# Kernel optimization log

Measured on AMD Instinct MI355X. Metric: run time of the kernel, lower is better.

## Reference

```python
import jax, jax.numpy as jnp
import numpy as np

B, S, D = 32, 512, 768
EPS = 1e-8  # torch CosineSimilarity eps

def setup_inputs() -> dict:
    key = jax.random.key(0)
    k1, k2, k3, k4 = jax.random.split(key, 4)
    emb1 = jax.random.normal(k1, (B, S, D), jnp.float32)
    emb2 = jax.random.normal(k2, (B, S, D), jnp.float32)
    mask1 = jax.random.randint(k3, (B, S), 0, 2).astype(jnp.int32)
    mask2 = jax.random.randint(k4, (B, S), 0, 2).astype(jnp.int32)
    return {"emb1": emb1, "emb2": emb2, "mask1": mask1, "mask2": mask2}

def reference(emb1, emb2, mask1, mask2):
    # normalize token embeddings (cosine sim = dot of unit vectors)
    n1 = emb1 / jnp.maximum(jnp.linalg.norm(emb1, axis=-1, keepdims=True), EPS)
    n2 = emb2 / jnp.maximum(jnp.linalg.norm(emb2, axis=-1, keepdims=True), EPS)
    # full pairwise cosine similarity: [B, S1, S2]
    sim = jnp.einsum('bid,bjd->bij', n1, n2)
    m1 = mask1.astype(sim.dtype)
    m2 = mask2.astype(sim.dtype)
    valid = m1[:, :, None] * m2[:, None, :]
    neg_inf = jnp.asarray(-jnp.inf, sim.dtype)
    masked = jnp.where(valid > 0, sim, neg_inf)
    # row max over valid cols; rows with no valid token contribute 0
    row_max = jnp.where(m1 > 0, jnp.max(masked, axis=2), 0.0)  # [B, S1]
    col_max = jnp.where(m2 > 0, jnp.max(masked, axis=1), 0.0)  # [B, S2]
    denom = jnp.sum(m1, axis=1) + jnp.sum(m2, axis=1)          # n1 + n2
    score = (jnp.sum(row_max, axis=1) + jnp.sum(col_max, axis=1)) / jnp.maximum(denom, 1.0)
    return score  # [B]
```

## Files before the change

kernel.cpp:

```cpp
#include <hip/hip_runtime.h>

#define BB 32
#define SS 512
#define DD 768
#define NROW (BB * SS)

typedef float f32x4 __attribute__((ext_vector_type(4)));
typedef short bf16x8 __attribute__((ext_vector_type(8)));

__device__ __forceinline__ unsigned fkey(float f) {
  unsigned u = __float_as_uint(f);
  return (u & 0x80000000u) ? ~u : (u | 0x80000000u);
}
__device__ __forceinline__ float fdecode(unsigned k) {
  return __uint_as_float((k & 0x80000000u) ? (k & 0x7fffffffu) : ~k);
}
__device__ __forceinline__ unsigned short cvt_bf16(float f) {
  unsigned u = __float_as_uint(f);
  u += 0x7fffu + ((u >> 16) & 1u);
  return (unsigned short)(u >> 16);
}

__global__ __launch_bounds__(64) void index_kernel(
    const int* __restrict__ mask1, const int* __restrict__ mask2,
    int* __restrict__ idx1, int* __restrict__ idx2,
    int* __restrict__ nt1, int* __restrict__ nt2,
    unsigned* __restrict__ rowkey, unsigned* __restrict__ colkey) {
  int side = blockIdx.x & 1, b = blockIdx.x >> 1;
  const int* m = (side ? mask2 : mask1) + b * SS;
  unsigned* key = (side ? colkey : rowkey) + b * SS;
  int* idx = (side ? idx2 : idx1) + b * SS;
  int l = threadIdx.x;
  int nv = 0, lastelem = 0;
#pragma unroll
  for (int c = 0; c < 8; ++c) {
    int e = c * 64 + l;
    int v = m[e];
    key[e] = 0x007fffffu;
    unsigned long long bal = __ballot(v != 0);
    int pos = nv + __popcll(bal & ((1ull << l) - 1ull));
    if (v) idx[pos] = e;
    nv += __popcll(bal);
    if (bal) lastelem = c * 64 + (63 - __clzll(bal));
  }
  int nt = (nv + 127) >> 7;
  for (int p = nv + l; p < nt * 128; p += 64) idx[p] = lastelem;
  if (l == 0) (side ? nt2 : nt1)[b] = nt;
}

__global__ __launch_bounds__(256) void norm_cvt_kernel(
    const float* __restrict__ emb1, const float* __restrict__ emb2,
    const int* __restrict__ mask1, const int* __restrict__ mask2,
    unsigned short* __restrict__ wsA, unsigned short* __restrict__ wsB) {
  int wave = blockIdx.x * 4 + (threadIdx.x >> 6);
  int lane = threadIdx.x & 63;
  int half = wave >> 14;
  int r = wave & (NROW - 1);
  if ((half ? mask2 : mask1)[r] == 0) return;
  const float* src = (half ? emb2 : emb1) + (size_t)r * DD;
  float4 v[3];
  float s = 0.f;
#pragma unroll
  for (int q = 0; q < 3; ++q) {
    v[q] = ((const float4*)src)[q * 64 + lane];
    s += v[q].x * v[q].x + v[q].y * v[q].y + v[q].z * v[q].z + v[q].w * v[q].w;
  }
#pragma unroll
  for (int m = 1; m < 64; m <<= 1) s += __shfl_xor(s, m);
  float inv = 1.0f / fmaxf(sqrtf(s), 1e-8f);
  unsigned short* dst = (half ? wsB : wsA) + (size_t)r * DD;
#pragma unroll
  for (int q = 0; q < 3; ++q) {
    ushort4 u;
    u.x = cvt_bf16(v[q].x * inv); u.y = cvt_bf16(v[q].y * inv);
    u.z = cvt_bf16(v[q].z * inv); u.w = cvt_bf16(v[q].w * inv);
    *(ushort4*)(dst + q * 256 + lane * 4) = u;
  }
}

__global__ __launch_bounds__(256) void simmax_kernel(
    const unsigned short* __restrict__ wsA, const unsigned short* __restrict__ wsB,
    const int* __restrict__ idx1, const int* __restrict__ idx2,
    const int* __restrict__ nt1, const int* __restrict__ nt2,
    unsigned* __restrict__ rowkey, unsigned* __restrict__ colkey) {
  int x = blockIdx.x;
  int b = x & 31;
  int tile = x >> 5;
  int ti = tile >> 2, tj = tile & 3;
  if (ti >= nt1[b] || tj >= nt2[b]) return;
  int i0 = ti << 7, j0 = tj << 7;
  __shared__ __align__(16) unsigned short sA[2][128 * 64];
  __shared__ __align__(16) unsigned short sB[2][128 * 64];
  int t = threadIdx.x, l = t & 63, wid = t >> 6, wr = wid >> 1, wc = wid & 1;
  int rsub = l >> 3, csub = l & 7;
  int ra[4], rb[4];
#pragma unroll
  for (int j = 0; j < 4; ++j) {
    int rowblk = (wid * 4 + j) * 8;
    ra[j] = idx1[b * SS + i0 + rowblk + rsub];
    rb[j] = idx2[b * SS + j0 + rowblk + rsub];
  }
  const unsigned short* gA = wsA + (size_t)b * SS * DD;
  const unsigned short* gB = wsB + (size_t)b * SS * DD;
  int csw = (csub ^ rsub) << 3;

  f32x4 acc[4][4] = {};

#define STAGE(buf, k0)                                                              \
  {                                                                                 \
    _Pragma("unroll") for (int j = 0; j < 4; ++j) {                                 \
      int rowblk = (wid * 4 + j) * 8;                                               \
      const unsigned short* ga = gA + (size_t)ra[j] * DD + (k0) + csw;              \
      const unsigned short* gb = gB + (size_t)rb[j] * DD + (k0) + csw;              \
      __builtin_amdgcn_global_load_lds(                                             \
          (const __attribute__((address_space(1))) unsigned int*)ga,                \
          (__attribute__((address_space(3))) unsigned int*)&sA[buf][rowblk * 64],   \
          16, 0, 0);                                                                \
      __builtin_amdgcn_global_load_lds(                                             \
          (const __attribute__((address_space(1))) unsigned int*)gb,                \
          (__attribute__((address_space(3))) unsigned int*)&sB[buf][rowblk * 64],   \
          16, 0, 0);                                                                \
    }                                                                               \
  }

  STAGE(0, 0);
  __syncthreads();
  int cur = 0;
#pragma unroll 1
  for (int tk = 0; tk < 12; ++tk) {
    if (tk < 11) STAGE(cur ^ 1, (tk + 1) * 64);
#pragma unroll
    for (int kk = 0; kk < 2; ++kk) {
      bf16x8 af[4], bfr[4];
#pragma unroll
      for (int mi = 0; mi < 4; ++mi) {
        int r = wr * 64 + mi * 16 + (l & 15);
        int ch = (kk << 2) + (l >> 4);
        af[mi] = *(const bf16x8*)(&sA[cur][(r << 6) + ((ch ^ (r & 7)) << 3)]);
      }
#pragma unroll
      for (int ni = 0; ni < 4; ++ni) {
        int r = wc * 64 + ni * 16 + (l & 15);
        int ch = (kk << 2) + (l >> 4);
        bfr[ni] = *(const bf16x8*)(&sB[cur][(r << 6) + ((ch ^ (r & 7)) << 3)]);
      }
#pragma unroll
      for (int mi = 0; mi < 4; ++mi)
#pragma unroll
        for (int ni = 0; ni < 4; ++ni)
          acc[mi][ni] = __builtin_amdgcn_mfma_f32_16x16x32_bf16(af[mi], bfr[ni], acc[mi][ni], 0, 0, 0);
    }
    __syncthreads();
    cur ^= 1;
  }

  const float NEG = -__builtin_inff();
  float rmax[4][4], cmax[4];
#pragma unroll
  for (int mi = 0; mi < 4; ++mi)
#pragma unroll
    for (int rg = 0; rg < 4; ++rg) rmax[mi][rg] = NEG;
#pragma unroll
  for (int ni = 0; ni < 4; ++ni) cmax[ni] = NEG;

#pragma unroll
  for (int mi = 0; mi < 4; ++mi)
#pragma unroll
    for (int ni = 0; ni < 4; ++ni)
#pragma unroll
      for (int rg = 0; rg < 4; ++rg) {
        float v = acc[mi][ni][rg];
        rmax[mi][rg] = fmaxf(rmax[mi][rg], v);
        cmax[ni] = fmaxf(cmax[ni], v);
      }
#pragma unroll
  for (int mi = 0; mi < 4; ++mi)
#pragma unroll
    for (int rg = 0; rg < 4; ++rg) {
      float v = rmax[mi][rg];
      v = fmaxf(v, __shfl_xor(v, 1));
      v = fmaxf(v, __shfl_xor(v, 2));
      v = fmaxf(v, __shfl_xor(v, 4));
      v = fmaxf(v, __shfl_xor(v, 8));
      rmax[mi][rg] = v;
    }
#pragma unroll
  for (int ni = 0; ni < 4; ++ni) {
    float v = cmax[ni];
    v = fmaxf(v, __shfl_xor(v, 16));
    v = fmaxf(v, __shfl_xor(v, 32));
    cmax[ni] = v;
  }
  int selm = (l >> 2) & 3, selr = l & 3, seln = (l >> 4) & 3;
  float rv = rmax[0][0], cv = cmax[0];
#pragma unroll
  for (int mi = 0; mi < 4; ++mi)
#pragma unroll
    for (int rg = 0; rg < 4; ++rg)
      if (selm == mi && selr == rg) rv = rmax[mi][rg];
#pragma unroll
  for (int ni = 0; ni < 4; ++ni)
    if (seln == ni) cv = cmax[ni];
  int rl = selm * 16 + ((l >> 4) & 3) * 4 + selr;
  int cl = seln * 16 + (l & 15);
  int orow = idx1[b * SS + i0 + wr * 64 + rl];
  int ocol = idx2[b * SS + j0 + wc * 64 + cl];
  atomicMax(&rowkey[b * SS + orow], fkey(rv));
  atomicMax(&colkey[b * SS + ocol], fkey(cv));
}

__global__ __launch_bounds__(256) void finalize_kernel(
    const int* __restrict__ mask1, const int* __restrict__ mask2,
    const unsigned* __restrict__ rowkey, const unsigned* __restrict__ colkey,
    float* __restrict__ out) {
  int b = blockIdx.x, t = threadIdx.x;
  float sum = 0.f;
  int cnt = 0;
  for (int s = t; s < SS; s += 256) {
    if (mask1[b * SS + s]) { sum += fdecode(rowkey[b * SS + s]); cnt++; }
    if (mask2[b * SS + s]) { sum += fdecode(colkey[b * SS + s]); cnt++; }
  }
#pragma unroll
  for (int m = 1; m < 64; m <<= 1) {
    sum += __shfl_xor(sum, m);
    cnt += __shfl_xor(cnt, m);
  }
  __shared__ float sS[4];
  __shared__ int sC[4];
  int w = t >> 6, lane = t & 63;
  if (lane == 0) { sS[w] = sum; sC[w] = cnt; }
  __syncthreads();
  if (t == 0) {
    float T = sS[0] + sS[1] + sS[2] + sS[3];
    int C = sC[0] + sC[1] + sC[2] + sC[3];
    out[b] = T / fmaxf((float)C, 1.0f);
  }
}

extern "C" void kernel_launch(void* const* d_in, const int* in_sizes, int n_in,
                              void* d_out, int out_size, void* d_ws, size_t ws_size,
                              hipStream_t stream) {
  const float* emb1 = (const float*)d_in[0];
  const float* emb2 = (const float*)d_in[1];
  const int* mask1 = (const int*)d_in[2];
  const int* mask2 = (const int*)d_in[3];
  float* out = (float*)d_out;

  unsigned short* wsA = (unsigned short*)d_ws;
  unsigned short* wsB = wsA + (size_t)NROW * DD;
  unsigned* rowkey = (unsigned*)(wsB + (size_t)NROW * DD);
  unsigned* colkey = rowkey + NROW;
  int* idx1 = (int*)(colkey + NROW);
  int* idx2 = idx1 + NROW;
  int* nt1 = idx2 + NROW;
  int* nt2 = nt1 + BB;

  index_kernel<<<64, 64, 0, stream>>>(mask1, mask2, idx1, idx2, nt1, nt2, rowkey, colkey);
  norm_cvt_kernel<<<8192, 256, 0, stream>>>(emb1, emb2, mask1, mask2, wsA, wsB);
  simmax_kernel<<<512, 256, 0, stream>>>(wsA, wsB, idx1, idx2, nt1, nt2, rowkey, colkey);
  finalize_kernel<<<BB, 256, 0, stream>>>(mask1, mask2, rowkey, colkey, out);
}
```

Baseline: 152.8 us.

## Compact valid rows contiguously and use 256x256 tiles in similarity max kernel

The normalize/convert kernel now writes valid tokens compacted by their position in the index list, so the GEMM reads contiguous rows instead of gathering through idx. The similarity kernel grows from 128x128 tiles with 4 waves to 256x256 tiles with 8 waves, launched as 128 blocks, which doubles operand reuse per LDS load. Padding rows are clamped to the last valid row. Larger tiles use about 128KB of LDS and 32 accumulators per wave, and only about 128 blocks run on a GPU with many CUs, so occupancy and parallelism drop.

```diff
diff --git a/kernel.cpp b/kernel.cpp
--- a/kernel.cpp
+++ b/kernel.cpp
@@ -24,6 +24,7 @@
 __global__ __launch_bounds__(64) void index_kernel(
     const int* __restrict__ mask1, const int* __restrict__ mask2,
     int* __restrict__ idx1, int* __restrict__ idx2,
+    int* __restrict__ nv1, int* __restrict__ nv2,
     int* __restrict__ nt1, int* __restrict__ nt2,
     unsigned* __restrict__ rowkey, unsigned* __restrict__ colkey) {
   int side = blockIdx.x & 1, b = blockIdx.x >> 1;
@@ -31,7 +32,7 @@
   unsigned* key = (side ? colkey : rowkey) + b * SS;
   int* idx = (side ? idx2 : idx1) + b * SS;
   int l = threadIdx.x;
-  int nv = 0, lastelem = 0;
+  int nv = 0;
 #pragma unroll
   for (int c = 0; c < 8; ++c) {
     int e = c * 64 + l;
@@ -41,23 +42,27 @@
     int pos = nv + __popcll(bal & ((1ull << l) - 1ull));
     if (v) idx[pos] = e;
     nv += __popcll(bal);
-    if (bal) lastelem = c * 64 + (63 - __clzll(bal));
-  }
-  int nt = (nv + 127) >> 7;
-  for (int p = nv + l; p < nt * 128; p += 64) idx[p] = lastelem;
-  if (l == 0) (side ? nt2 : nt1)[b] = nt;
+  }
+  if (l == 0) {
+    (side ? nv2 : nv1)[b] = nv;
+    (side ? nt2 : nt1)[b] = (nv + 255) >> 8;
+  }
 }
 
 __global__ __launch_bounds__(256) void norm_cvt_kernel(
     const float* __restrict__ emb1, const float* __restrict__ emb2,
-    const int* __restrict__ mask1, const int* __restrict__ mask2,
+    const int* __restrict__ idx1, const int* __restrict__ idx2,
+    const int* __restrict__ nv1, const int* __restrict__ nv2,
     unsigned short* __restrict__ wsA, unsigned short* __restrict__ wsB) {
   int wave = blockIdx.x * 4 + (threadIdx.x >> 6);
   int lane = threadIdx.x & 63;
-  int half = wave >> 14;
-  int r = wave & (NROW - 1);
-  if ((half ? mask2 : mask1)[r] == 0) return;
-  const float* src = (half ? emb2 : emb1) + (size_t)r * DD;
+  int side = wave >> 14;
+  int pg = wave & 16383;
+  int b = pg >> 9, p = pg & 511;
+  int nv = (side ? nv2 : nv1)[b];
+  if (p >= nv) return;
+  int orig = (side ? idx2 : idx1)[b * SS + p];
+  const float* src = (side ? emb2 : emb1) + ((size_t)b * SS + orig) * DD;
   float4 v[3];
   float s = 0.f;
 #pragma unroll
@@ -68,7 +73,7 @@
 #pragma unroll
   for (int m = 1; m < 64; m <<= 1) s += __shfl_xor(s, m);
   float inv = 1.0f / fmaxf(sqrtf(s), 1e-8f);
-  unsigned short* dst = (half ? wsB : wsA) + (size_t)r * DD;
+  unsigned short* dst = (side ? wsB : wsA) + ((size_t)b * SS + p) * DD;
 #pragma unroll
   for (int q = 0; q < 3; ++q) {
     ushort4 u;
@@ -78,47 +83,50 @@
   }
 }
 
-__global__ __launch_bounds__(256) void simmax_kernel(
+__global__ __launch_bounds__(512, 1) void simmax_kernel(
     const unsigned short* __restrict__ wsA, const unsigned short* __restrict__ wsB,
     const int* __restrict__ idx1, const int* __restrict__ idx2,
+    const int* __restrict__ nv1, const int* __restrict__ nv2,
     const int* __restrict__ nt1, const int* __restrict__ nt2,
     unsigned* __restrict__ rowkey, unsigned* __restrict__ colkey) {
   int x = blockIdx.x;
   int b = x & 31;
   int tile = x >> 5;
-  int ti = tile >> 2, tj = tile & 3;
+  int ti = tile >> 1, tj = tile & 1;
   if (ti >= nt1[b] || tj >= nt2[b]) return;
-  int i0 = ti << 7, j0 = tj << 7;
-  __shared__ __align__(16) unsigned short sA[2][128 * 64];
-  __shared__ __align__(16) unsigned short sB[2][128 * 64];
-  int t = threadIdx.x, l = t & 63, wid = t >> 6, wr = wid >> 1, wc = wid & 1;
+  int NV1 = nv1[b], NV2 = nv2[b];
+  int i0 = ti << 8, j0 = tj << 8;
+  __shared__ __align__(16) unsigned short sA[2][256 * 64];
+  __shared__ __align__(16) unsigned short sB[2][256 * 64];
+  int t = threadIdx.x, l = t & 63, w = t >> 6, wr = w >> 2, wc = w & 3;
   int rsub = l >> 3, csub = l & 7;
-  int ra[4], rb[4];
-#pragma unroll
-  for (int j = 0; j < 4; ++j) {
-    int rowblk = (wid * 4 + j) * 8;
-    ra[j] = idx1[b * SS + i0 + rowblk + rsub];
-    rb[j] = idx2[b * SS + j0 + rowblk + rsub];
-  }
+  int csw = (csub ^ rsub) << 3;
   const unsigned short* gA = wsA + (size_t)b * SS * DD;
   const unsigned short* gB = wsB + (size_t)b * SS * DD;
-  int csw = (csub ^ rsub) << 3;
-
-  f32x4 acc[4][4] = {};
+  size_t offA[4], offB[4];
+#pragma unroll
+  for (int j = 0; j < 4; ++j) {
+    int rb_ = j * 64 + w * 8;
+    int pa = i0 + rb_ + rsub, pb = j0 + rb_ + rsub;
+    pa = pa < NV1 - 1 ? pa : NV1 - 1;
+    pb = pb < NV2 - 1 ? pb : NV2 - 1;
+    offA[j] = (size_t)pa * DD + csw;
+    offB[j] = (size_t)pb * DD + csw;
+  }
+
+  f32x4 acc[8][4] = {};
 
 #define STAGE(buf, k0)                                                              \
   {                                                                                 \
     _Pragma("unroll") for (int j = 0; j < 4; ++j) {                                 \
-      int rowblk = (wid * 4 + j) * 8;                                               \
-      const unsigned short* ga = gA + (size_t)ra[j] * DD + (k0) + csw;              \
-      const unsigned short* gb = gB + (size_t)rb[j] * DD + (k0) + csw;              \
+      int rb_ = j * 64 + w * 8;                                                     \
       __builtin_amdgcn_global_load_lds(                                             \
-          (const __attribute__((address_space(1))) unsigned int*)ga,                \
-          (__attribute__((address_space(3))) unsigned int*)&sA[buf][rowblk * 64],   \
+          (const __attribute__((address_space(1))) unsigned int*)(gA + offA[j] + (k0)), \
+          (__attribute__((address_space(3))) unsigned int*)&sA[buf][rb_ * 64],      \
           16, 0, 0);                                                                \
       __builtin_amdgcn_global_load_lds(                                             \
-          (const __attribute__((address_space(1))) unsigned int*)gb,                \
-          (__attribute__((address_space(3))) unsigned int*)&sB[buf][rowblk * 64],   \
+          (const __attribute__((address_space(1))) unsigned int*)(gB + offB[j] + (k0)), \
+          (__attribute__((address_space(3))) unsigned int*)&sB[buf][rb_ * 64],      \
           16, 0, 0);                                                                \
     }                                                                               \
   }
@@ -131,10 +139,10 @@
     if (tk < 11) STAGE(cur ^ 1, (tk + 1) * 64);
 #pragma unroll
     for (int kk = 0; kk < 2; ++kk) {
-      bf16x8 af[4], bfr[4];
-#pragma unroll
-      for (int mi = 0; mi < 4; ++mi) {
-        int r = wr * 64 + mi * 16 + (l & 15);
+      bf16x8 af[8], bfv[4];
+#pragma unroll
+      for (int mi = 0; mi < 8; ++mi) {
+        int r = wr * 128 + mi * 16 + (l & 15);
         int ch = (kk << 2) + (l >> 4);
         af[mi] = *(const bf16x8*)(&sA[cur][(r << 6) + ((ch ^ (r & 7)) << 3)]);
       }
@@ -142,29 +150,29 @@
       for (int ni = 0; ni < 4; ++ni) {
         int r = wc * 64 + ni * 16 + (l & 15);
         int ch = (kk << 2) + (l >> 4);
-        bfr[ni] = *(const bf16x8*)(&sB[cur][(r << 6) + ((ch ^ (r & 7)) << 3)]);
-      }
-#pragma unroll
-      for (int mi = 0; mi < 4; ++mi)
+        bfv[ni] = *(const bf16x8*)(&sB[cur][(r << 6) + ((ch ^ (r & 7)) << 3)]);
+      }
+#pragma unroll
+      for (int mi = 0; mi < 8; ++mi)
 #pragma unroll
         for (int ni = 0; ni < 4; ++ni)
-          acc[mi][ni] = __builtin_amdgcn_mfma_f32_16x16x32_bf16(af[mi], bfr[ni], acc[mi][ni], 0, 0, 0);
+          acc[mi][ni] = __builtin_amdgcn_mfma_f32_16x16x32_bf16(af[mi], bfv[ni], acc[mi][ni], 0, 0, 0);
     }
     __syncthreads();
     cur ^= 1;
   }
 
   const float NEG = -__builtin_inff();
-  float rmax[4][4], cmax[4];
-#pragma unroll
-  for (int mi = 0; mi < 4; ++mi)
+  float rmax[8][4], cmax[4];
+#pragma unroll
+  for (int mi = 0; mi < 8; ++mi)
 #pragma unroll
     for (int rg = 0; rg < 4; ++rg) rmax[mi][rg] = NEG;
 #pragma unroll
   for (int ni = 0; ni < 4; ++ni) cmax[ni] = NEG;
 
 #pragma unroll
-  for (int mi = 0; mi < 4; ++mi)
+  for (int mi = 0; mi < 8; ++mi)
 #pragma unroll
     for (int ni = 0; ni < 4; ++ni)
 #pragma unroll
@@ -174,7 +182,7 @@
         cmax[ni] = fmaxf(cmax[ni], v);
       }
 #pragma unroll
-  for (int mi = 0; mi < 4; ++mi)
+  for (int mi = 0; mi < 8; ++mi)
 #pragma unroll
     for (int rg = 0; rg < 4; ++rg) {
       float v = rmax[mi][rg];
@@ -191,22 +199,26 @@
     v = fmaxf(v, __shfl_xor(v, 32));
     cmax[ni] = v;
   }
-  int selm = (l >> 2) & 3, selr = l & 3, seln = (l >> 4) & 3;
-  float rv = rmax[0][0], cv = cmax[0];
-#pragma unroll
-  for (int mi = 0; mi < 4; ++mi)
-#pragma unroll
-    for (int rg = 0; rg < 4; ++rg)
-      if (selm == mi && selr == rg) rv = rmax[mi][rg];
-#pragma unroll
-  for (int ni = 0; ni < 4; ++ni)
-    if (seln == ni) cv = cmax[ni];
-  int rl = selm * 16 + ((l >> 4) & 3) * 4 + selr;
-  int cl = seln * 16 + (l & 15);
-  int orow = idx1[b * SS + i0 + wr * 64 + rl];
-  int ocol = idx2[b * SS + j0 + wc * 64 + cl];
-  atomicMax(&rowkey[b * SS + orow], fkey(rv));
-  atomicMax(&colkey[b * SS + ocol], fkey(cv));
+#pragma unroll
+  for (int mi = 0; mi < 8; ++mi)
+#pragma unroll
+    for (int rg = 0; rg < 4; ++rg) {
+      if (((mi * 4 + rg) & 15) == (l & 15)) {
+        int p = i0 + wr * 128 + mi * 16 + ((l >> 4) << 2) + rg;
+        p = p < NV1 - 1 ? p : NV1 - 1;
+        int orow = idx1[b * SS + p];
+        atomicMax(&rowkey[b * SS + orow], fkey(rmax[mi][rg]));
+      }
+    }
+#pragma unroll
+  for (int ni = 0; ni < 4; ++ni) {
+    if ((l >> 4) == ni) {
+      int p = j0 + wc * 64 + ni * 16 + (l & 15);
+      p = p < NV2 - 1 ? p : NV2 - 1;
+      int ocol = idx2[b * SS + p];
+      atomicMax(&colkey[b * SS + ocol], fkey(cmax[ni]));
+    }
+  }
 }
 
 __global__ __launch_bounds__(256) void finalize_kernel(
@@ -252,11 +264,13 @@
   unsigned* colkey = rowkey + NROW;
   int* idx1 = (int*)(colkey + NROW);
   int* idx2 = idx1 + NROW;
-  int* nt1 = idx2 + NROW;
+  int* nv1 = idx2 + NROW;
+  int* nv2 = nv1 + BB;
+  int* nt1 = nv2 + BB;
   int* nt2 = nt1 + BB;
 
-  index_kernel<<<64, 64, 0, stream>>>(mask1, mask2, idx1, idx2, nt1, nt2, rowkey, colkey);
-  norm_cvt_kernel<<<8192, 256, 0, stream>>>(emb1, emb2, mask1, mask2, wsA, wsB);
-  simmax_kernel<<<512, 256, 0, stream>>>(wsA, wsB, idx1, idx2, nt1, nt2, rowkey, colkey);
+  index_kernel<<<64, 64, 0, stream>>>(mask1, mask2, idx1, idx2, nv1, nv2, nt1, nt2, rowkey, colkey);
+  norm_cvt_kernel<<<8192, 256, 0, stream>>>(emb1, emb2, idx1, idx2, nv1, nv2, wsA, wsB);
+  simmax_kernel<<<128, 512, 0, stream>>>(wsA, wsB, idx1, idx2, nv1, nv2, nt1, nt2, rowkey, colkey);
   finalize_kernel<<<BB, 256, 0, stream>>>(mask1, mask2, rowkey, colkey, out);
 }
```

Measured after the change: 181.3 us. 1.19x slower.

## Store normalized bf16 rows compacted by valid-token position instead of original index

Applied to the files above, without the earlier changes.

The normalization kernel now gathers only valid tokens through the index list and writes them contiguously into the workspace. The similarity kernel then reads contiguous rows directly, clamping padding rows to the last valid one, instead of doing a scattered gather per tile. This is meant to improve memory locality and drop the indirection in the GEMM loads. The cost is an extra dependent index load in the normalization kernel and new per-batch count arrays.

```diff
diff --git a/kernel.cpp b/kernel.cpp
--- a/kernel.cpp
+++ b/kernel.cpp
@@ -24,6 +24,7 @@
 __global__ __launch_bounds__(64) void index_kernel(
     const int* __restrict__ mask1, const int* __restrict__ mask2,
     int* __restrict__ idx1, int* __restrict__ idx2,
+    int* __restrict__ nv1, int* __restrict__ nv2,
     int* __restrict__ nt1, int* __restrict__ nt2,
     unsigned* __restrict__ rowkey, unsigned* __restrict__ colkey) {
   int side = blockIdx.x & 1, b = blockIdx.x >> 1;
@@ -31,7 +32,7 @@
   unsigned* key = (side ? colkey : rowkey) + b * SS;
   int* idx = (side ? idx2 : idx1) + b * SS;
   int l = threadIdx.x;
-  int nv = 0, lastelem = 0;
+  int nv = 0;
 #pragma unroll
   for (int c = 0; c < 8; ++c) {
     int e = c * 64 + l;
@@ -41,23 +42,27 @@
     int pos = nv + __popcll(bal & ((1ull << l) - 1ull));
     if (v) idx[pos] = e;
     nv += __popcll(bal);
-    if (bal) lastelem = c * 64 + (63 - __clzll(bal));
-  }
-  int nt = (nv + 127) >> 7;
-  for (int p = nv + l; p < nt * 128; p += 64) idx[p] = lastelem;
-  if (l == 0) (side ? nt2 : nt1)[b] = nt;
+  }
+  if (l == 0) {
+    (side ? nv2 : nv1)[b] = nv;
+    (side ? nt2 : nt1)[b] = (nv + 127) >> 7;
+  }
 }
 
 __global__ __launch_bounds__(256) void norm_cvt_kernel(
     const float* __restrict__ emb1, const float* __restrict__ emb2,
-    const int* __restrict__ mask1, const int* __restrict__ mask2,
+    const int* __restrict__ idx1, const int* __restrict__ idx2,
+    const int* __restrict__ nv1, const int* __restrict__ nv2,
     unsigned short* __restrict__ wsA, unsigned short* __restrict__ wsB) {
   int wave = blockIdx.x * 4 + (threadIdx.x >> 6);
   int lane = threadIdx.x & 63;
-  int half = wave >> 14;
-  int r = wave & (NROW - 1);
-  if ((half ? mask2 : mask1)[r] == 0) return;
-  const float* src = (half ? emb2 : emb1) + (size_t)r * DD;
+  int side = wave >> 14;
+  int pg = wave & 16383;
+  int b = pg >> 9, p = pg & 511;
+  int nv = (side ? nv2 : nv1)[b];
+  if (p >= nv) return;
+  int orig = (side ? idx2 : idx1)[b * SS + p];
+  const float* src = (side ? emb2 : emb1) + ((size_t)b * SS + orig) * DD;
   float4 v[3];
   float s = 0.f;
 #pragma unroll
@@ -68,7 +73,7 @@
 #pragma unroll
   for (int m = 1; m < 64; m <<= 1) s += __shfl_xor(s, m);
   float inv = 1.0f / fmaxf(sqrtf(s), 1e-8f);
-  unsigned short* dst = (half ? wsB : wsA) + (size_t)r * DD;
+  unsigned short* dst = (side ? wsB : wsA) + ((size_t)b * SS + p) * DD;
 #pragma unroll
   for (int q = 0; q < 3; ++q) {
     ushort4 u;
@@ -81,6 +86,7 @@
 __global__ __launch_bounds__(256) void simmax_kernel(
     const unsigned short* __restrict__ wsA, const unsigned short* __restrict__ wsB,
     const int* __restrict__ idx1, const int* __restrict__ idx2,
+    const int* __restrict__ nv1, const int* __restrict__ nv2,
     const int* __restrict__ nt1, const int* __restrict__ nt2,
     unsigned* __restrict__ rowkey, unsigned* __restrict__ colkey) {
   int x = blockIdx.x;
@@ -88,39 +94,41 @@
   int tile = x >> 5;
   int ti = tile >> 2, tj = tile & 3;
   if (ti >= nt1[b] || tj >= nt2[b]) return;
+  int NV1 = nv1[b], NV2 = nv2[b];
   int i0 = ti << 7, j0 = tj << 7;
   __shared__ __align__(16) unsigned short sA[2][128 * 64];
   __shared__ __align__(16) unsigned short sB[2][128 * 64];
   int t = threadIdx.x, l = t & 63, wid = t >> 6, wr = wid >> 1, wc = wid & 1;
   int rsub = l >> 3, csub = l & 7;
-  int ra[4], rb[4];
+  int csw = (csub ^ rsub) << 3;
+  const unsigned short* gA = wsA + (size_t)b * SS * DD;
+  const unsigned short* gB = wsB + (size_t)b * SS * DD;
+  size_t offA[4], offB[4];
 #pragma unroll
   for (int j = 0; j < 4; ++j) {
     int rowblk = (wid * 4 + j) * 8;
-    ra[j] = idx1[b * SS + i0 + rowblk + rsub];
-    rb[j] = idx2[b * SS + j0 + rowblk + rsub];
-  }
-  const unsigned short* gA = wsA + (size_t)b * SS * DD;
-  const unsigned short* gB = wsB + (size_t)b * SS * DD;
-  int csw = (csub ^ rsub) << 3;
+    int pa = i0 + rowblk + rsub, pb = j0 + rowblk + rsub;
+    pa = pa < NV1 - 1 ? pa : NV1 - 1;
+    pb = pb < NV2 - 1 ? pb : NV2 - 1;
+    offA[j] = (size_t)pa * DD + csw;
+    offB[j] = (size_t)pb * DD + csw;
+  }
 
   f32x4 acc[4][4] = {};
 
-#define STAGE(buf, k0)                                                              \
-  {                                                                                 \
-    _Pragma("unroll") for (int j = 0; j < 4; ++j) {                                 \
-      int rowblk = (wid * 4 + j) * 8;                                               \
-      const unsigned short* ga = gA + (size_t)ra[j] * DD + (k0) + csw;              \
-      const unsigned short* gb = gB + (size_t)rb[j] * DD + (k0) + csw;              \
-      __builtin_amdgcn_global_load_lds(                                             \
-          (const __attribute__((address_space(1))) unsigned int*)ga,                \
-          (__attribute__((address_space(3))) unsigned int*)&sA[buf][rowblk * 64],   \
-          16, 0, 0);                                                                \
-      __builtin_amdgcn_global_load_lds(                                             \
-          (const __attribute__((address_space(1))) unsigned int*)gb,                \
-          (__attribute__((address_space(3))) unsigned int*)&sB[buf][rowblk * 64],   \
-          16, 0, 0);                                                                \
-    }                                                                               \
+#define STAGE(buf, k0)                                                                  \
+  {                                                                                     \
+    _Pragma("unroll") for (int j = 0; j < 4; ++j) {                                     \
+      int rowblk = (wid * 4 + j) * 8;                                                   \
+      __builtin_amdgcn_global_load_lds(                                                 \
+          (const __attribute__((address_space(1))) unsigned int*)(gA + offA[j] + (k0)), \
+          (__attribute__((address_space(3))) unsigned int*)&sA[buf][rowblk * 64],       \
+          16, 0, 0);                                                                    \
+      __builtin_amdgcn_global_load_lds(                                                 \
+          (const __attribute__((address_space(1))) unsigned int*)(gB + offB[j] + (k0)), \
+          (__attribute__((address_space(3))) unsigned int*)&sB[buf][rowblk * 64],       \
+          16, 0, 0);                                                                    \
+    }                                                                                   \
   }
 
   STAGE(0, 0);
@@ -131,7 +139,7 @@
     if (tk < 11) STAGE(cur ^ 1, (tk + 1) * 64);
 #pragma unroll
     for (int kk = 0; kk < 2; ++kk) {
-      bf16x8 af[4], bfr[4];
+      bf16x8 af[4], bfv[4];
 #pragma unroll
       for (int mi = 0; mi < 4; ++mi) {
         int r = wr * 64 + mi * 16 + (l & 15);
@@ -142,13 +150,13 @@
       for (int ni = 0; ni < 4; ++ni) {
         int r = wc * 64 + ni * 16 + (l & 15);
         int ch = (kk << 2) + (l >> 4);
-        bfr[ni] = *(const bf16x8*)(&sB[cur][(r << 6) + ((ch ^ (r & 7)) << 3)]);
+        bfv[ni] = *(const bf16x8*)(&sB[cur][(r << 6) + ((ch ^ (r & 7)) << 3)]);
       }
 #pragma unroll
       for (int mi = 0; mi < 4; ++mi)
 #pragma unroll
         for (int ni = 0; ni < 4; ++ni)
-          acc[mi][ni] = __builtin_amdgcn_mfma_f32_16x16x32_bf16(af[mi], bfr[ni], acc[mi][ni], 0, 0, 0);
+          acc[mi][ni] = __builtin_amdgcn_mfma_f32_16x16x32_bf16(af[mi], bfv[ni], acc[mi][ni], 0, 0, 0);
     }
     __syncthreads();
     cur ^= 1;
@@ -203,8 +211,12 @@
     if (seln == ni) cv = cmax[ni];
   int rl = selm * 16 + ((l >> 4) & 3) * 4 + selr;
   int cl = seln * 16 + (l & 15);
-  int orow = idx1[b * SS + i0 + wr * 64 + rl];
-  int ocol = idx2[b * SS + j0 + wc * 64 + cl];
+  int pr = i0 + wr * 64 + rl;
+  pr = pr < NV1 - 1 ? pr : NV1 - 1;
+  int pc = j0 + wc * 64 + cl;
+  pc = pc < NV2 - 1 ? pc : NV2 - 1;
+  int orow = idx1[b * SS + pr];
+  int ocol = idx2[b * SS + pc];
   atomicMax(&rowkey[b * SS + orow], fkey(rv));
   atomicMax(&colkey[b * SS + ocol], fkey(cv));
 }
@@ -252,11 +264,13 @@
   unsigned* colkey = rowkey + NROW;
   int* idx1 = (int*)(colkey + NROW);
   int* idx2 = idx1 + NROW;
-  int* nt1 = idx2 + NROW;
+  int* nv1 = idx2 + NROW;
+  int* nv2 = nv1 + BB;
+  int* nt1 = nv2 + BB;
   int* nt2 = nt1 + BB;
 
-  index_kernel<<<64, 64, 0, stream>>>(mask1, mask2, idx1, idx2, nt1, nt2, rowkey, colkey);
-  norm_cvt_kernel<<<8192, 256, 0, stream>>>(emb1, emb2, mask1, mask2, wsA, wsB);
-  simmax_kernel<<<512, 256, 0, stream>>>(wsA, wsB, idx1, idx2, nt1, nt2, rowkey, colkey);
+  index_kernel<<<64, 64, 0, stream>>>(mask1, mask2, idx1, idx2, nv1, nv2, nt1, nt2, rowkey, colkey);
+  norm_cvt_kernel<<<8192, 256, 0, stream>>>(emb1, emb2, idx1, idx2, nv1, nv2, wsA, wsB);
+  simmax_kernel<<<512, 256, 0, stream>>>(wsA, wsB, idx1, idx2, nv1, nv2, nt1, nt2, rowkey, colkey);
   finalize_kernel<<<BB, 256, 0, stream>>>(mask1, mask2, rowkey, colkey, out);
 }
```

Result: no change. 153.1 us (+0.2%).
